# Optimization experiments

Hardware: AMD Instinct MI355X
Metric: run time of the kernel (lower is better)

The kernel has to match this reference:

```python
import jax, jax.numpy as jnp
import numpy as np

N_NODES = 50000
N_EDGES = 640000
IN_C = 128
HID = 128


def gcn_conv(x, edge_index, W, b):
    """PyG GCNConv: out = D^-1/2 (A + I) D^-1/2 (x @ W) + b, with self-loops added."""
    n = x.shape[0]
    loop = jnp.arange(n, dtype=edge_index.dtype)
    src = jnp.concatenate([edge_index[0], loop])  # [E+N]
    dst = jnp.concatenate([edge_index[1], loop])
    # degree of each node counting self-loop, computed on destination side
    deg = jax.ops.segment_sum(jnp.ones_like(dst, dtype=x.dtype), dst, num_segments=n)
    dinv = jnp.where(deg > 0, jax.lax.rsqrt(deg), 0.0)
    norm = dinv[src] * dinv[dst]  # [E+N]
    h = x @ W                      # transform first (cheaper than post-aggregation when in>=out)
    msg = h[src] * norm[:, None]   # gather + normalize  [E+N, HID]
    out = jax.ops.segment_sum(msg, dst, num_segments=n)  # scatter-add
    return out + b


def setup_inputs() -> dict:
    key = jax.random.key(0)
    ks = jax.random.split(key, 8)
    x = jax.random.normal(ks[0], (N_NODES, IN_C), dtype=jnp.float32)
    edge_index = jax.random.randint(ks[1], (2, N_EDGES), 0, N_NODES, dtype=jnp.int64)
    s_in = 1.0 / np.sqrt(IN_C)
    s_h = 1.0 / np.sqrt(HID)
    s_l = 1.0 / np.sqrt(2 * HID)
    W1 = jax.random.normal(ks[2], (IN_C, HID), dtype=jnp.float32) * s_in
    b1 = jnp.zeros((HID,), dtype=jnp.float32)
    W2 = jax.random.normal(ks[3], (HID, HID), dtype=jnp.float32) * s_h
    b2 = jnp.zeros((HID,), dtype=jnp.float32)
    Wlin = jax.random.normal(ks[4], (2 * HID, HID), dtype=jnp.float32) * s_l
    blin = jax.random.normal(ks[5], (HID,), dtype=jnp.float32) * s_l
    return {"x": x, "edge_index": edge_index, "W1": W1, "b1": b1,
            "W2": W2, "b2": b2, "Wlin": Wlin, "blin": blin}


def reference(x, edge_index, W1, b1, W2, b2, Wlin, blin):
    x1 = jax.nn.relu(gcn_conv(x, edge_index, W1, b1))
    x2 = jax.nn.relu(gcn_conv(x1, edge_index, W2, b2))
    out = jnp.concatenate([x1, x2], axis=-1) @ Wlin + blin
    return out
```

## Files before the change

kernel.cpp:

```cpp
#include <hip/hip_runtime.h>


#define THREADS 256
#define NCHUNK 64
#define RN     12544
#define CPAD   50176

typedef unsigned int uint;
typedef __attribute__((ext_vector_type(8))) _Float16 half8v;
typedef __attribute__((ext_vector_type(2))) _Float16 half2v;
typedef __attribute__((ext_vector_type(4))) float f32x4;

__device__ __forceinline__ int edge_at(const int* e32, const long long* e64,
                                       int is64, long long idx) {
    return is64 ? (int)e64[idx] : e32[idx];
}

__device__ __forceinline__ size_t fragidx(int k, int ncol) {
    int ks = k >> 5, fg = (k >> 3) & 3, i = k & 7;
    int n = ncol >> 4, fr = ncol & 15;
    return ((size_t)(ks * 8 + n) * 512) + (size_t)(fg * 16 + fr) * 8 + i;
}

__global__ void prep_kernel(const unsigned int* e, int* flag,
                            const float* __restrict__ W1, const float* __restrict__ W2,
                            const float* __restrict__ WL,
                            _Float16* __restrict__ F1, _Float16* __restrict__ F2,
                            _Float16* __restrict__ FL) {
    int i = blockIdx.x * blockDim.x + threadIdx.x;
    if (i == 0) flag[1] = 0;
    if (blockIdx.x == 0 && threadIdx.x < 64) {
        unsigned int v = (threadIdx.x < 32) ? e[2 * threadIdx.x + 1] : 0u;
        unsigned long long b = __ballot(v != 0u);
        if (threadIdx.x == 0) flag[0] = (b == 0ull) ? 1 : 0;
    }
    if (i < 65536) {
        const float* W; _Float16* F; int j;
        if (i < 16384)      { W = W1; F = F1; j = i; }
        else if (i < 32768) { W = W2; F = F2; j = i - 16384; }
        else                { W = WL; F = FL; j = i - 32768; }
        int k = j >> 7, n = j & 127;
        F[fragidx(k, n)] = (_Float16)W[j];
    }
}

__device__ __forceinline__ half8v loadA8(const _Float16* p) {
    return *(const half8v*)p;
}
__device__ __forceinline__ half8v loadA8(const float* p) {
    float4 v0 = *(const float4*)p;
    float4 v1 = *(const float4*)(p + 4);
    half8v o = {(_Float16)v0.x, (_Float16)v0.y, (_Float16)v0.z, (_Float16)v0.w,
                (_Float16)v1.x, (_Float16)v1.y, (_Float16)v1.z, (_Float16)v1.w};
    return o;
}

template <int K, typename AT, typename OT>
__device__ __forceinline__ void mgemm_body(
        int bid, _Float16* ws,
        const AT* __restrict__ A, int lda,
        const _Float16* __restrict__ Wf,
        const float* __restrict__ bias,
        OT* __restrict__ C, int ldc, int M) {
    constexpr int NK = K >> 5;
    int tid = threadIdx.x;
    int lane = tid & 63;
    int w = tid >> 6;
    int fr = lane & 15;
    int fg = lane >> 4;
    int kb = fg * 8;
    int rowW = bid * 64 + w * 16;

    int arow = rowW + fr;
    if (arow >= M) arow = M - 1;
    half8v a[NK];
    #pragma unroll
    for (int ks = 0; ks < NK; ++ks)
        a[ks] = loadA8(A + (size_t)arow * lda + ks * 32 + kb);

    {
        constexpr int SW = K / 16;
        const uint4* src = (const uint4*)Wf;
        uint4* dst = (uint4*)ws;
        uint4 tmp[SW];
        #pragma unroll
        for (int s = 0; s < SW; ++s) tmp[s] = src[tid + 256 * s];
        #pragma unroll
        for (int s = 0; s < SW; ++s) dst[tid + 256 * s] = tmp[s];
    }
    __syncthreads();

    f32x4 acc[8];
    #pragma unroll
    for (int n = 0; n < 8; ++n) acc[n] = (f32x4){0.f, 0.f, 0.f, 0.f};

    #pragma unroll
    for (int ks = 0; ks < NK; ++ks) {
        #pragma unroll
        for (int n = 0; n < 8; ++n) {
            half8v bh = *(const half8v*)(ws + (size_t)(ks * 8 + n) * 512 + lane * 8);
            acc[n] = __builtin_amdgcn_mfma_f32_16x16x32_f16(a[ks], bh, acc[n], 0, 0, 0);
        }
    }

    int crow = fg * 4;
    #pragma unroll
    for (int r = 0; r < 4; ++r) {
        int row = rowW + crow + r;
        if (row < M) {
            #pragma unroll
            for (int n = 0; n < 8; ++n) {
                int c = n * 16 + fr;
                float v = acc[n][r];
                if (bias) v += bias[c];
                C[(size_t)row * ldc + c] = (OT)v;
            }
        }
    }
}

template <int K, typename AT, typename OT>
__global__ __launch_bounds__(256, (K > 128 ? 2 : 3)) void mgemm_kernel(
        const AT* __restrict__ A, int lda,
        const _Float16* __restrict__ Wf, const float* __restrict__ bias,
        OT* __restrict__ C, int ldc, int M) {
    constexpr int NK = K >> 5;
    __shared__ _Float16 ws[NK * 8 * 512];
    mgemm_body<K, AT, OT>(blockIdx.x, ws, A, lda, Wf, bias, C, ldc, M);
}

__device__ __forceinline__ void count_body(
        int abid, uint* lcnt,
        const int* e32, const long long* e64, const int* flag,
        int E, int* counts, int N) {
    int chunk = abid >> 2, range = abid & 3;
    int nbase = range * RN;
    int rn = N - nbase; if (rn > RN) rn = RN;
    int tid = threadIdx.x;
    for (int i = tid; i < RN; i += THREADS) lcnt[i] = 0u;
    __syncthreads();
    int is64 = flag[0];
    int CH = (E + NCHUNK - 1) / NCHUNK;
    int e0 = chunk * CH;
    int e1 = e0 + CH; if (e1 > E) e1 = E;
    for (int i = e0 + tid; i < e1; i += THREADS) {
        int d = edge_at(e32, e64, is64, (long long)E + i);
        uint r = (uint)(d - nbase);
        if (r < (uint)rn) atomicAdd(&lcnt[r], 1u);
    }
    __syncthreads();
    for (int i = tid; i < rn; i += THREADS)
        counts[(size_t)chunk * CPAD + nbase + i] = (int)lcnt[i];
}

__global__ __launch_bounds__(256, 3) void mgemm_count_kernel(
        const float* __restrict__ A, const _Float16* __restrict__ Wf,
        _Float16* __restrict__ C, int M, int GB,
        const int* e32, const long long* e64, const int* flag,
        int E, int* counts, int N) {
    __shared__ alignas(16) unsigned char shbuf[RN * 4];
    int bid = blockIdx.x;
    if (bid < GB) {
        mgemm_body<128, float, _Float16>(bid, (_Float16*)shbuf, A, 128, Wf,
                                         nullptr, C, 128, M);
    } else {
        count_body(bid - GB, (uint*)shbuf, e32, e64, flag, E, counts, N);
    }
}

__global__ void prefix_kernel(int* __restrict__ counts, int* __restrict__ rowptr,
                              int* __restrict__ cnt, float* __restrict__ dinv,
                              int* cursor, int N) {
    int n = blockIdx.x * blockDim.x + threadIdx.x;
    int lane = threadIdx.x & 63;
    int s = 0;
    if (n < N) {
        #pragma unroll 4
        for (int c = 0; c < NCHUNK; ++c) {
            size_t idx = (size_t)c * CPAD + n;
            int v = counts[idx];
            counts[idx] = s;
            s += v;
        }
        cnt[n] = s;
        dinv[n] = rsqrtf((float)(s + 1));
    }
    int pre = s;
    #pragma unroll
    for (int d = 1; d < 64; d <<= 1) {
        int v = __shfl_up(pre, d);
        if (lane >= d) pre += v;
    }
    int wavesum = __shfl(pre, 63);
    int base = 0;
    if (lane == 63) base = atomicAdd(cursor, wavesum);
    base = __shfl(base, 63);
    if (n < N) rowptr[n] = base + pre - s;
}

__global__ __launch_bounds__(256, 3) void place_kernel(
        const int* e32, const long long* e64, const int* flag, int E,
        const int* __restrict__ counts, const int* __restrict__ rowptr,
        int* __restrict__ col, int N) {
    __shared__ uint lptr[RN];
    int abid = blockIdx.x;
    int chunk = abid >> 2, range = abid & 3;
    int nbase = range * RN;
    int rn = N - nbase; if (rn > RN) rn = RN;
    int tid = threadIdx.x;
    for (int i = tid; i < rn; i += THREADS)
        lptr[i] = (uint)(counts[(size_t)chunk * CPAD + nbase + i] + rowptr[nbase + i]);
    __syncthreads();
    int is64 = flag[0];
    int CH = (E + NCHUNK - 1) / NCHUNK;
    int e0 = chunk * CH;
    int e1 = e0 + CH; if (e1 > E) e1 = E;
    for (int i = e0 + tid; i < e1; i += THREADS) {
        int d = edge_at(e32, e64, is64, (long long)E + i);
        uint r = (uint)(d - nbase);
        if (r < (uint)rn) {
            int s = edge_at(e32, e64, is64, i);
            uint slot = atomicAdd(&lptr[r], 1u);
            col[slot] = s;
        }
    }
}

__global__ __launch_bounds__(256) void agg_kernel(
        const _Float16* __restrict__ h, const int* __restrict__ rowptr,
        const int* __restrict__ cnt, const int* __restrict__ col,
        const float* __restrict__ dinv, const float* __restrict__ bias,
        _Float16* __restrict__ out, int ldo, int N) {
    int node = blockIdx.x * 4 + (threadIdx.x >> 6);
    if (node >= N) return;
    int lane = threadIdx.x & 63;

    float di = dinv[node];
    float wself = di * di;
    half2v v = ((const half2v*)(h + (size_t)node * 128))[lane];
    float ax0 = (float)v[0] * wself, ay0 = (float)v[1] * wself;
    float ax1 = 0.f, ay1 = 0.f, ax2 = 0.f, ay2 = 0.f, ax3 = 0.f, ay3 = 0.f;

    int p = rowptr[node];
    int en = p + cnt[node];
    for (; p + 7 < en; p += 8) {
        int s0 = col[p],     s1 = col[p + 1], s2 = col[p + 2], s3 = col[p + 3];
        int s4 = col[p + 4], s5 = col[p + 5], s6 = col[p + 6], s7 = col[p + 7];
        float w0 = dinv[s0] * di, w1 = dinv[s1] * di;
        float w2 = dinv[s2] * di, w3 = dinv[s3] * di;
        float w4 = dinv[s4] * di, w5 = dinv[s5] * di;
        float w6 = dinv[s6] * di, w7 = dinv[s7] * di;
        half2v h0 = ((const half2v*)(h + (size_t)s0 * 128))[lane];
        half2v h1 = ((const half2v*)(h + (size_t)s1 * 128))[lane];
        half2v h2 = ((const half2v*)(h + (size_t)s2 * 128))[lane];
        half2v h3 = ((const half2v*)(h + (size_t)s3 * 128))[lane];
        half2v h4 = ((const half2v*)(h + (size_t)s4 * 128))[lane];
        half2v h5 = ((const half2v*)(h + (size_t)s5 * 128))[lane];
        half2v h6 = ((const half2v*)(h + (size_t)s6 * 128))[lane];
        half2v h7 = ((const half2v*)(h + (size_t)s7 * 128))[lane];
        ax0 += (float)h0[0] * w0; ay0 += (float)h0[1] * w0;
        ax1 += (float)h1[0] * w1; ay1 += (float)h1[1] * w1;
        ax2 += (float)h2[0] * w2; ay2 += (float)h2[1] * w2;
        ax3 += (float)h3[0] * w3; ay3 += (float)h3[1] * w3;
        ax0 += (float)h4[0] * w4; ay0 += (float)h4[1] * w4;
        ax1 += (float)h5[0] * w5; ay1 += (float)h5[1] * w5;
        ax2 += (float)h6[0] * w6; ay2 += (float)h6[1] * w6;
        ax3 += (float)h7[0] * w7; ay3 += (float)h7[1] * w7;
    }
    for (; p + 3 < en; p += 4) {
        int s0 = col[p], s1 = col[p + 1], s2 = col[p + 2], s3 = col[p + 3];
        float w0 = dinv[s0] * di, w1 = dinv[s1] * di;
        float w2 = dinv[s2] * di, w3 = dinv[s3] * di;
        half2v h0 = ((const half2v*)(h + (size_t)s0 * 128))[lane];
        half2v h1 = ((const half2v*)(h + (size_t)s1 * 128))[lane];
        half2v h2 = ((const half2v*)(h + (size_t)s2 * 128))[lane];
        half2v h3 = ((const half2v*)(h + (size_t)s3 * 128))[lane];
        ax0 += (float)h0[0] * w0; ay0 += (float)h0[1] * w0;
        ax1 += (float)h1[0] * w1; ay1 += (float)h1[1] * w1;
        ax2 += (float)h2[0] * w2; ay2 += (float)h2[1] * w2;
        ax3 += (float)h3[0] * w3; ay3 += (float)h3[1] * w3;
    }
    for (; p < en; ++p) {
        int s0 = col[p];
        float w0 = dinv[s0] * di;
        half2v h0 = ((const half2v*)(h + (size_t)s0 * 128))[lane];
        ax0 += (float)h0[0] * w0; ay0 += (float)h0[1] * w0;
    }
    float ax = (ax0 + ax1) + (ax2 + ax3) + bias[2 * lane];
    float ay = (ay0 + ay1) + (ay2 + ay3) + bias[2 * lane + 1];
    ax = fmaxf(ax, 0.f);
    ay = fmaxf(ay, 0.f);
    half2v o = {(_Float16)ax, (_Float16)ay};
    ((half2v*)(out + (size_t)node * ldo))[lane] = o;
}

extern "C" void kernel_launch(void* const* d_in, const int* in_sizes, int n_in,
                              void* d_out, int out_size, void* d_ws, size_t ws_size,
                              hipStream_t stream) {
    const float* x    = (const float*)d_in[0];
    const void*  edges = d_in[1];
    const float* W1   = (const float*)d_in[2];
    const float* b1   = (const float*)d_in[3];
    const float* W2   = (const float*)d_in[4];
    const float* b2   = (const float*)d_in[5];
    const float* Wlin = (const float*)d_in[6];
    const float* blin = (const float*)d_in[7];
    float* out = (float*)d_out;

    const int C = 128;
    int N = in_sizes[0] / C;
    int E = in_sizes[1] / 2;

    char* w = (char*)d_ws;
    auto carve = [&](size_t bytes) {
        char* p = w;
        w += (bytes + 255) & ~(size_t)255;
        return (void*)p;
    };
    int*   flag   = (int*)carve(256);
    int*   cnt    = (int*)carve((size_t)N * 4);
    int*   rowptr = (int*)carve((size_t)N * 4);
    float* dinv   = (float*)carve((size_t)N * 4);
    int*   counts = (int*)carve((size_t)NCHUNK * CPAD * 4);
    int*   col    = (int*)carve((size_t)E * 4);
    _Float16* h   = (_Float16*)carve((size_t)N * 128 * 2);
    _Float16* xc  = (_Float16*)carve((size_t)N * 256 * 2);
    _Float16* F1  = (_Float16*)carve((size_t)128 * 128 * 2);
    _Float16* F2  = (_Float16*)carve((size_t)128 * 128 * 2);
    _Float16* FL  = (_Float16*)carve((size_t)256 * 128 * 2);

    const int* e32 = (const int*)edges;
    const long long* e64 = (const long long*)edges;

    int gemm_grid = (N + 63) / 64;
    int abc_grid  = NCHUNK * 4;
    int agg_grid  = (N + 3) / 4;

    prep_kernel<<<256, THREADS, 0, stream>>>(
        (const unsigned int*)edges, flag, W1, W2, Wlin, F1, F2, FL);

    mgemm_count_kernel<<<gemm_grid + abc_grid, THREADS, 0, stream>>>(
        x, F1, h, N, gemm_grid, e32, e64, flag, E, counts, N);

    prefix_kernel<<<(N + THREADS - 1) / THREADS, THREADS, 0, stream>>>(
        counts, rowptr, cnt, dinv, flag + 1, N);

    place_kernel<<<abc_grid, THREADS, 0, stream>>>(
        e32, e64, flag, E, counts, rowptr, col, N);

    agg_kernel<<<agg_grid, 256, 0, stream>>>(h, rowptr, cnt, col, dinv, b1, xc, 256, N);
    mgemm_kernel<128, _Float16, _Float16><<<gemm_grid, 256, 0, stream>>>(
        xc, 256, F2, nullptr, h, 128, N);
    agg_kernel<<<agg_grid, 256, 0, stream>>>(h, rowptr, cnt, col, dinv, b2, xc + 128, 256, N);
    mgemm_kernel<256, _Float16, float><<<gemm_grid, 256, 0, stream>>>(
        xc, 256, FL, blin, out, 128, N);
}
```

Before: 244.2 us.

## Fuse aggregation with following GEMMs and pack degree counts into 16-bit halves

Merges each neighbor-aggregation pass with the GEMM that consumes it. Each block aggregates 64 nodes into a swizzled LDS tile, then runs MFMA against the weight fragments held in LDS, so the intermediate activations no longer go through global memory. This removes two launches and the xc round trip, but the gather phase now runs at GEMM-style occupancy with 64-node blocks instead of the small 4-node blocks, which may hurt latency hiding for the irregular gathers. Separately, the count pass packs two 16-bit counters per LDS word, which halves the chunk-by-range grid and the edge re-reads. That assumes no node gets 65536 or more in-edges from a single chunk.

```diff
diff --git a/kernel.cpp b/kernel.cpp
--- a/kernel.cpp
+++ b/kernel.cpp
@@ -4,6 +4,8 @@
 #define THREADS 256
 #define NCHUNK 64
 #define RN     12544
+#define RN2    25088
+#define HRN    12544
 #define CPAD   50176
 
 typedef unsigned int uint;
@@ -119,25 +121,15 @@
     }
 }
 
-template <int K, typename AT, typename OT>
-__global__ __launch_bounds__(256, (K > 128 ? 2 : 3)) void mgemm_kernel(
-        const AT* __restrict__ A, int lda,
-        const _Float16* __restrict__ Wf, const float* __restrict__ bias,
-        OT* __restrict__ C, int ldc, int M) {
-    constexpr int NK = K >> 5;
-    __shared__ _Float16 ws[NK * 8 * 512];
-    mgemm_body<K, AT, OT>(blockIdx.x, ws, A, lda, Wf, bias, C, ldc, M);
-}
-
 __device__ __forceinline__ void count_body(
         int abid, uint* lcnt,
         const int* e32, const long long* e64, const int* flag,
         int E, int* counts, int N) {
-    int chunk = abid >> 2, range = abid & 3;
-    int nbase = range * RN;
-    int rn = N - nbase; if (rn > RN) rn = RN;
+    int chunk = abid >> 1, range = abid & 1;
+    int nbase = range * RN2;
+    int rn = N - nbase; if (rn > RN2) rn = RN2;
     int tid = threadIdx.x;
-    for (int i = tid; i < RN; i += THREADS) lcnt[i] = 0u;
+    for (int i = tid; i < HRN; i += THREADS) lcnt[i] = 0u;
     __syncthreads();
     int is64 = flag[0];
     int CH = (E + NCHUNK - 1) / NCHUNK;
@@ -146,11 +138,12 @@
     for (int i = e0 + tid; i < e1; i += THREADS) {
         int d = edge_at(e32, e64, is64, (long long)E + i);
         uint r = (uint)(d - nbase);
-        if (r < (uint)rn) atomicAdd(&lcnt[r], 1u);
+        if (r < (uint)rn) atomicAdd(&lcnt[r >> 1], 1u << ((r & 1) * 16));
     }
     __syncthreads();
     for (int i = tid; i < rn; i += THREADS)
-        counts[(size_t)chunk * CPAD + nbase + i] = (int)lcnt[i];
+        counts[(size_t)chunk * CPAD + nbase + i] =
+            (int)((lcnt[i >> 1] >> ((i & 1) * 16)) & 0xffffu);
 }
 
 __global__ __launch_bounds__(256, 3) void mgemm_count_kernel(
@@ -158,7 +151,7 @@
         _Float16* __restrict__ C, int M, int GB,
         const int* e32, const long long* e64, const int* flag,
         int E, int* counts, int N) {
-    __shared__ alignas(16) unsigned char shbuf[RN * 4];
+    __shared__ alignas(16) unsigned char shbuf[HRN * 4];
     int bid = blockIdx.x;
     if (bid < GB) {
         mgemm_body<128, float, _Float16>(bid, (_Float16*)shbuf, A, 128, Wf,
@@ -226,15 +219,11 @@
     }
 }
 
-__global__ __launch_bounds__(256) void agg_kernel(
+__device__ __forceinline__ void agg_node(
         const _Float16* __restrict__ h, const int* __restrict__ rowptr,
         const int* __restrict__ cnt, const int* __restrict__ col,
         const float* __restrict__ dinv, const float* __restrict__ bias,
-        _Float16* __restrict__ out, int ldo, int N) {
-    int node = blockIdx.x * 4 + (threadIdx.x >> 6);
-    if (node >= N) return;
-    int lane = threadIdx.x & 63;
-
+        int node, int lane, float& rax, float& ray) {
     float di = dinv[node];
     float wself = di * di;
     half2v v = ((const half2v*)(h + (size_t)node * 128))[lane];
@@ -288,10 +277,158 @@
     }
     float ax = (ax0 + ax1) + (ax2 + ax3) + bias[2 * lane];
     float ay = (ay0 + ay1) + (ay2 + ay3) + bias[2 * lane + 1];
-    ax = fmaxf(ax, 0.f);
-    ay = fmaxf(ay, 0.f);
-    half2v o = {(_Float16)ax, (_Float16)ay};
-    ((half2v*)(out + (size_t)node * ldo))[lane] = o;
+    rax = fmaxf(ax, 0.f);
+    ray = fmaxf(ay, 0.f);
+}
+
+__device__ __forceinline__ void xa_store(_Float16* xa, int r, int lane, half2v o) {
+    *(half2v*)((char*)xa + r * 256 + ((lane * 4) ^ ((r & 7) << 4))) = o;
+}
+__device__ __forceinline__ half8v xa_load(const _Float16* xa, int r, int colbyte) {
+    return *(const half8v*)((const char*)xa + r * 256 + (colbyte ^ ((r & 7) << 4)));
+}
+
+__global__ __launch_bounds__(256, 3) void agg_gemm_kernel(
+        const _Float16* __restrict__ h1, const int* __restrict__ rowptr,
+        const int* __restrict__ cnt, const int* __restrict__ col,
+        const float* __restrict__ dinv, const float* __restrict__ b1,
+        _Float16* __restrict__ x1, const _Float16* __restrict__ F2,
+        _Float16* __restrict__ h2, int N) {
+    __shared__ _Float16 ws[4 * 8 * 512];
+    __shared__ _Float16 xa[64 * 128];
+    int tid = threadIdx.x;
+    int lane = tid & 63;
+    int w = tid >> 6;
+    int fr = lane & 15, fg = lane >> 4;
+    int bid = blockIdx.x;
+
+    {
+        const uint4* src = (const uint4*)F2;
+        uint4* dst = (uint4*)ws;
+        uint4 tmp[8];
+        #pragma unroll
+        for (int s = 0; s < 8; ++s) tmp[s] = src[tid + 256 * s];
+        #pragma unroll
+        for (int s = 0; s < 8; ++s) dst[tid + 256 * s] = tmp[s];
+    }
+    for (int i = 0; i < 16; ++i) {
+        int r = w * 16 + i;
+        int node = bid * 64 + r;
+        if (node < N) {
+            float ax, ay;
+            agg_node(h1, rowptr, cnt, col, dinv, b1, node, lane, ax, ay);
+            half2v o = {(_Float16)ax, (_Float16)ay};
+            ((half2v*)(x1 + (size_t)node * 128))[lane] = o;
+            xa_store(xa, r, lane, o);
+        }
+    }
+    __syncthreads();
+
+    f32x4 acc[8];
+    #pragma unroll
+    for (int n = 0; n < 8; ++n) acc[n] = (f32x4){0.f, 0.f, 0.f, 0.f};
+    int r2 = w * 16 + fr;
+    half8v a[4];
+    #pragma unroll
+    for (int ks = 0; ks < 4; ++ks)
+        a[ks] = xa_load(xa, r2, ks * 64 + fg * 16);
+    #pragma unroll
+    for (int ks = 0; ks < 4; ++ks) {
+        #pragma unroll
+        for (int n = 0; n < 8; ++n) {
+            half8v bh = *(const half8v*)(ws + (size_t)(ks * 8 + n) * 512 + lane * 8);
+            acc[n] = __builtin_amdgcn_mfma_f32_16x16x32_f16(a[ks], bh, acc[n], 0, 0, 0);
+        }
+    }
+    int rowW = bid * 64 + w * 16;
+    int crow = fg * 4;
+    #pragma unroll
+    for (int r = 0; r < 4; ++r) {
+        int row = rowW + crow + r;
+        if (row < N) {
+            #pragma unroll
+            for (int n = 0; n < 8; ++n)
+                h2[(size_t)row * 128 + n * 16 + fr] = (_Float16)acc[n][r];
+        }
+    }
+}
+
+__global__ __launch_bounds__(256, 2) void agg_head_kernel(
+        const _Float16* __restrict__ h2, const int* __restrict__ rowptr,
+        const int* __restrict__ cnt, const int* __restrict__ col,
+        const float* __restrict__ dinv, const float* __restrict__ b2,
+        const _Float16* __restrict__ x1, const _Float16* __restrict__ FL,
+        const float* __restrict__ blin, float* __restrict__ out, int N) {
+    __shared__ _Float16 ws[8 * 8 * 512];
+    __shared__ _Float16 xa[64 * 128];
+    int tid = threadIdx.x;
+    int lane = tid & 63;
+    int w = tid >> 6;
+    int fr = lane & 15, fg = lane >> 4;
+    int kb = fg * 8;
+    int bid = blockIdx.x;
+
+    int arow = bid * 64 + w * 16 + fr;
+    if (arow >= N) arow = N - 1;
+    half8v a[8];
+    #pragma unroll
+    for (int ks = 0; ks < 4; ++ks)
+        a[ks] = loadA8(x1 + (size_t)arow * 128 + ks * 32 + kb);
+
+    {
+        const uint4* src = (const uint4*)FL;
+        uint4* dst = (uint4*)ws;
+        uint4 tmp[8];
+        #pragma unroll
+        for (int s = 0; s < 8; ++s) tmp[s] = src[tid + 256 * s];
+        #pragma unroll
+        for (int s = 0; s < 8; ++s) dst[tid + 256 * s] = tmp[s];
+        #pragma unroll
+        for (int s = 0; s < 8; ++s) tmp[s] = src[tid + 256 * (8 + s)];
+        #pragma unroll
+        for (int s = 0; s < 8; ++s) dst[tid + 256 * (8 + s)] = tmp[s];
+    }
+    for (int i = 0; i < 16; ++i) {
+        int r = w * 16 + i;
+        int node = bid * 64 + r;
+        if (node < N) {
+            float ax, ay;
+            agg_node(h2, rowptr, cnt, col, dinv, b2, node, lane, ax, ay);
+            half2v o = {(_Float16)ax, (_Float16)ay};
+            xa_store(xa, r, lane, o);
+        }
+    }
+    __syncthreads();
+
+    int r2 = w * 16 + fr;
+    #pragma unroll
+    for (int ks = 0; ks < 4; ++ks)
+        a[4 + ks] = xa_load(xa, r2, ks * 64 + fg * 16);
+
+    f32x4 acc[8];
+    #pragma unroll
+    for (int n = 0; n < 8; ++n) acc[n] = (f32x4){0.f, 0.f, 0.f, 0.f};
+    #pragma unroll
+    for (int ks = 0; ks < 8; ++ks) {
+        #pragma unroll
+        for (int n = 0; n < 8; ++n) {
+            half8v bh = *(const half8v*)(ws + (size_t)(ks * 8 + n) * 512 + lane * 8);
+            acc[n] = __builtin_amdgcn_mfma_f32_16x16x32_f16(a[ks], bh, acc[n], 0, 0, 0);
+        }
+    }
+    int rowW = bid * 64 + w * 16;
+    int crow = fg * 4;
+    #pragma unroll
+    for (int r = 0; r < 4; ++r) {
+        int row = rowW + crow + r;
+        if (row < N) {
+            #pragma unroll
+            for (int n = 0; n < 8; ++n) {
+                int c = n * 16 + fr;
+                out[(size_t)row * 128 + c] = acc[n][r] + blin[c];
+            }
+        }
+    }
 }
 
 extern "C" void kernel_launch(void* const* d_in, const int* in_sizes, int n_in,
@@ -323,8 +460,9 @@
     float* dinv   = (float*)carve((size_t)N * 4);
     int*   counts = (int*)carve((size_t)NCHUNK * CPAD * 4);
     int*   col    = (int*)carve((size_t)E * 4);
-    _Float16* h   = (_Float16*)carve((size_t)N * 128 * 2);
-    _Float16* xc  = (_Float16*)carve((size_t)N * 256 * 2);
+    _Float16* h1  = (_Float16*)carve((size_t)N * 128 * 2);
+    _Float16* h2  = (_Float16*)carve((size_t)N * 128 * 2);
+    _Float16* x1  = (_Float16*)carve((size_t)N * 128 * 2);
     _Float16* F1  = (_Float16*)carve((size_t)128 * 128 * 2);
     _Float16* F2  = (_Float16*)carve((size_t)128 * 128 * 2);
     _Float16* FL  = (_Float16*)carve((size_t)256 * 128 * 2);
@@ -332,26 +470,25 @@
     const int* e32 = (const int*)edges;
     const long long* e64 = (const long long*)edges;
 
-    int gemm_grid = (N + 63) / 64;
-    int abc_grid  = NCHUNK * 4;
-    int agg_grid  = (N + 3) / 4;
+    int gemm_grid  = (N + 63) / 64;
+    int count_grid = NCHUNK * 2;
+    int place_grid = NCHUNK * 4;
 
     prep_kernel<<<256, THREADS, 0, stream>>>(
         (const unsigned int*)edges, flag, W1, W2, Wlin, F1, F2, FL);
 
-    mgemm_count_kernel<<<gemm_grid + abc_grid, THREADS, 0, stream>>>(
-        x, F1, h, N, gemm_grid, e32, e64, flag, E, counts, N);
+    mgemm_count_kernel<<<gemm_grid + count_grid, THREADS, 0, stream>>>(
+        x, F1, h1, N, gemm_grid, e32, e64, flag, E, counts, N);
 
     prefix_kernel<<<(N + THREADS - 1) / THREADS, THREADS, 0, stream>>>(
         counts, rowptr, cnt, dinv, flag + 1, N);
 
-    place_kernel<<<abc_grid, THREADS, 0, stream>>>(
+    place_kernel<<<place_grid, THREADS, 0, stream>>>(
         e32, e64, flag, E, counts, rowptr, col, N);
 
-    agg_kernel<<<agg_grid, 256, 0, stream>>>(h, rowptr, cnt, col, dinv, b1, xc, 256, N);
-    mgemm_kernel<128, _Float16, _Float16><<<gemm_grid, 256, 0, stream>>>(
-        xc, 256, F2, nullptr, h, 128, N);
-    agg_kernel<<<agg_grid, 256, 0, stream>>>(h, rowptr, cnt, col, dinv, b2, xc + 128, 256, N);
-    mgemm_kernel<256, _Float16, float><<<gemm_grid, 256, 0, stream>>>(
-        xc, 256, FL, blin, out, 128, N);
-}
+    agg_gemm_kernel<<<gemm_grid, THREADS, 0, stream>>>(
+        h1, rowptr, cnt, col, dinv, b1, x1, F2, h2, N);
+
+    agg_head_kernel<<<gemm_grid, THREADS, 0, stream>>>(
+        h2, rowptr, cnt, col, dinv, b2, x1, FL, blin, out, N);
+}
```

Result: slower. 336.1 us (+37.6%).
